# Kernel optimization log

Measured on AMD Instinct MI355X. Metric: run time of the kernel, lower is better.

## Reference

```python
import jax, jax.numpy as jnp
import numpy as np

B, D, O = 32768, 512, 16          # batch, input_size, output_size
E, K, T = 16, 4, 3                # n_expert, top-k, n_task
H1, H2 = 16, 8                    # Expert hidden sizes (hard-coded in Expert)
SPARSE_COEF, OLMO_COEF, RZ_COEF = 0.01, 0.01, 0.001


def setup_inputs() -> dict:
    key = jax.random.key(0)
    ks = jax.random.split(key, 8)
    s = 0.05
    return {
        "x": jax.random.normal(ks[0], (B, D), jnp.float32),
        # per-task gate params (torch inits zeros; random here for a meaningful test)
        "w_gates": jax.random.normal(ks[1], (T, D, E), jnp.float32) * s,
        "b_gates": jnp.zeros((T, E), jnp.float32),
        # stacked expert MLP params: Linear(D,16)->ReLU->Linear(16,8)->ReLU->Linear(8,O)->ReLU
        "W1": jax.random.normal(ks[2], (E, D, H1), jnp.float32) * s,
        "b1": jnp.zeros((E, H1), jnp.float32),
        "W2": jax.random.normal(ks[3], (E, H1, H2), jnp.float32) * s,
        "b2": jnp.zeros((E, H2), jnp.float32),
        "W3": jax.random.normal(ks[4], (E, H2, O), jnp.float32) * s,
        "b3": jnp.zeros((E, O), jnp.float32),
    }


def cv_squared(v):
    # torch .var() is unbiased (ddof=1)
    eps = 1e-10
    return jnp.var(v, ddof=1) / (jnp.mean(v) ** 2 + eps)


def reference(x, w_gates, b_gates, W1, b1, W2, b2, W3, b3):
    Bn = x.shape[0]
    # router z loss uses raw input x (as in the source)
    rz_per_task = jnp.sum(jax.nn.logsumexp(x, axis=-1)) / Bn

    # All experts on all samples, vectorized over the expert axis.
    # (experts are identical across tasks, so compute once; gating makes it sparse)
    h1 = jax.nn.relu(jnp.einsum('bd,edh->ebh', x, W1) + b1[:, None, :])   # [E,B,16]
    h2 = jax.nn.relu(jnp.einsum('ebh,ehk->ebk', h1, W2) + b2[:, None, :])  # [E,B,8]
    eo = jax.nn.relu(jnp.einsum('ebk,eko->ebo', h2, W3) + b3[:, None, :])  # [E,B,O]

    row = jnp.arange(Bn)[:, None]
    ys = []
    lb_loss = jnp.float32(0.0)
    rz_loss = jnp.float32(0.0)
    for t in range(T):  # small fixed task loop
        logits = x @ w_gates[t] + b_gates[t]               # [B,E]
        top_vals, top_idx = jax.lax.top_k(logits, K)
        top_gates = jax.nn.softmax(top_vals, axis=1)
        gates = jnp.zeros_like(logits).at[row, top_idx].set(top_gates)  # [B,E]

        load = (gates > 0).sum(0).astype(jnp.float32)      # eval-mode load
        importance = gates.sum(0)
        sparse_lb = cv_squared(importance) + cv_squared(load)
        olmo_lb = E * jnp.sum(importance * (load / Bn))
        lb_loss = lb_loss + sparse_lb * SPARSE_COEF + olmo_lb * OLMO_COEF
        rz_loss = rz_loss + rz_per_task * RZ_COEF

        # combine: y[b] = sum_e gates[b,e] * expert_e(x[b])
        ys.append(jnp.einsum('be,ebo->bo', gates, eo))
    return (jnp.stack(ys), lb_loss, rz_loss)
```

## Files before the change

### kernel.cpp

```cpp
#include <hip/hip_runtime.h>
#include <hip/hip_bf16.h>

#define BSZ 32768
#define TT  3
#define OO  16

typedef __attribute__((ext_vector_type(8))) short bf16x8;
typedef __attribute__((ext_vector_type(4))) float f32x4;

__device__ __forceinline__ float bf2f(unsigned short u) {
  return __uint_as_float(((unsigned)u) << 16);
}
__device__ __forceinline__ unsigned short f2bf(float f) {
  unsigned u = __float_as_uint(f);
  u += 0x7fffu + ((u >> 16) & 1u);
  return (unsigned short)(u >> 16);
}
__device__ __forceinline__ unsigned pack2(unsigned short a, unsigned short b) {
  return (unsigned)a | ((unsigned)b << 16);
}

__global__ void k_prepw(const float* __restrict__ W1, const float* __restrict__ wg,
                        unsigned short* __restrict__ Wfh,
                        unsigned short* __restrict__ Wfl, float* __restrict__ acc) {
  if (blockIdx.x == 0 && threadIdx.x < 97) acc[threadIdx.x] = 0.f;
  for (int idx = blockIdx.x * 256 + threadIdx.x; idx < 20 * 16 * 64 * 8;
       idx += gridDim.x * 256) {
    const int nblk = idx >> 13, itg = (idx >> 9) & 15;
    const int lane = (idx >> 3) & 63, j = idx & 7;
    const int n = nblk * 16 + (lane & 15);
    const int k = itg * 32 + (lane >> 4) * 8 + j;
    float v = 0.f;
    if (n < 256) v = W1[(size_t)(n >> 4) * 8192 + k * 16 + (n & 15)];
    else if (n < 304) v = wg[(size_t)((n - 256) >> 4) * 8192 + k * 16 + ((n - 256) & 15)];
    const unsigned short hi = f2bf(v);
    Wfh[idx] = hi;
    Wfl[idx] = f2bf(v - bf2f(hi));
  }
}

struct FSmem {
  union {
    struct {
      unsigned short xh[4][4][64][8];
      unsigned short xl[4][4][64][8];
    } a;
    struct {
      unsigned short hd[16][264];
      float eoL[16][16][17];
      float gvL[64][12];
      int   giL[64][12];
      union {
        float lgs[64][52];
        struct { float W2t[2048], W3t[2048]; } t;
      } u2;
      float b2t[128], b3t[256];
      float impL[48], loadL[48];
      int   nresc, resc[192];
      double resL[16];
    } b;
  } u;
  float rzrow[64];
};

__global__ __launch_bounds__(512, 4) void k_fused(
    const float* __restrict__ x, const unsigned short* __restrict__ Wfh,
    const unsigned short* __restrict__ Wfl, const float* __restrict__ b1,
    const float* __restrict__ bg, const float* __restrict__ wg,
    const float* __restrict__ W2, const float* __restrict__ b2,
    const float* __restrict__ W3, const float* __restrict__ b3,
    float* __restrict__ out, float* __restrict__ acc_imp,
    float* __restrict__ acc_load, float* __restrict__ rz_acc) {
  __shared__ FSmem sm;
  const int tid = threadIdx.x;
  const int b0 = blockIdx.x * 64;
  const int w = tid >> 6, l = tid & 63;
  const int l15 = l & 15, quad = l >> 4;
  const int mh = w >> 2;
  const int cg = w & 3;
  const int srow = tid >> 3, skf = tid & 7;
  const int sm_abs = srow >> 4;
  const int slane = (srow & 15) + 16 * (skf >> 1);
  const int sj = (skf & 1) * 4;

  f32x4 acc[2][5];
#pragma unroll
  for (int m = 0; m < 2; m++)
#pragma unroll
    for (int c = 0; c < 5; c++) acc[m][c] = (f32x4){0.f, 0.f, 0.f, 0.f};
  float rzsum = 0.f;

  auto woffs = [&](int itg, int c) -> size_t {
    return ((size_t)(((cg * 5 + c) * 16 + itg) * 64 + l)) * 8;
  };

#pragma unroll 1
  for (int ch = 0; ch < 4; ++ch) {
    if (ch) __syncthreads();
    {
      float4 xv[4];
      const float* xp = &x[(size_t)(b0 + srow) * 512 + ch * 128 + skf * 4];
#pragma unroll
      for (int r = 0; r < 4; r++) xv[r] = *(const float4*)(xp + r * 32);
#pragma unroll
      for (int r = 0; r < 4; r++) {
        const float v0 = xv[r].x, v1 = xv[r].y, v2 = xv[r].z, v3 = xv[r].w;
        rzsum += __expf(v0) + __expf(v1) + __expf(v2) + __expf(v3);
        const unsigned short h0 = f2bf(v0), h1_ = f2bf(v1), h2_ = f2bf(v2), h3 = f2bf(v3);
        uint2 ph, pl;
        ph.x = pack2(h0, h1_); ph.y = pack2(h2_, h3);
        pl.x = pack2(f2bf(v0 - bf2f(h0)), f2bf(v1 - bf2f(h1_)));
        pl.y = pack2(f2bf(v2 - bf2f(h2_)), f2bf(v3 - bf2f(h3)));
        *(uint2*)&sm.u.a.xh[sm_abs][r][slane][sj] = ph;
        *(uint2*)&sm.u.a.xl[sm_abs][r][slane][sj] = pl;
      }
    }
    __syncthreads();

    bf16x8 bh = *(const bf16x8*)&Wfh[woffs(ch * 4, 0)];
    bf16x8 bl = *(const bf16x8*)&Wfl[woffs(ch * 4, 0)];
#pragma unroll
    for (int it = 0; it < 4; ++it) {
      bf16x8 ah[2], al[2];
#pragma unroll
      for (int m = 0; m < 2; m++) {
        ah[m] = *(const bf16x8*)&sm.u.a.xh[mh * 2 + m][it][l][0];
        al[m] = *(const bf16x8*)&sm.u.a.xl[mh * 2 + m][it][l][0];
      }
#pragma unroll
      for (int c = 0; c < 5; c++) {
        bf16x8 bhn = bh, bln = bl;
        if (!((it == 3) && (c == 4))) {
          const int nit = (c == 4) ? it + 1 : it;
          const int nc  = (c == 4) ? 0 : c + 1;
          const size_t o = woffs(ch * 4 + nit, nc);
          bhn = *(const bf16x8*)&Wfh[o];
          bln = *(const bf16x8*)&Wfl[o];
        }
#pragma unroll
        for (int m = 0; m < 2; m++) {
          acc[m][c] = __builtin_amdgcn_mfma_f32_16x16x32_bf16(ah[m], bh, acc[m][c], 0, 0, 0);
          acc[m][c] = __builtin_amdgcn_mfma_f32_16x16x32_bf16(al[m], bh, acc[m][c], 0, 0, 0);
          acc[m][c] = __builtin_amdgcn_mfma_f32_16x16x32_bf16(ah[m], bl, acc[m][c], 0, 0, 0);
        }
        bh = bhn; bl = bln;
      }
    }
  }

  rzsum += __shfl_xor(rzsum, 1);
  rzsum += __shfl_xor(rzsum, 2);
  rzsum += __shfl_xor(rzsum, 4);
  if (skf == 0) sm.rzrow[srow] = rzsum;
  __syncthreads();

  if (tid < 64) {
    float vv = __logf(sm.rzrow[tid]);
#pragma unroll
    for (int off = 32; off; off >>= 1) vv += __shfl_xor(vv, off);
    if (tid == 0) atomicAdd(rz_acc, vv);
  }
  if (cg == 3) {
#pragma unroll
    for (int c = 1; c < 4; c++) {
      const int cc = 16 * c + l15 - 16;
#pragma unroll
      for (int m = 0; m < 2; m++)
#pragma unroll
        for (int reg = 0; reg < 4; reg++) {
          const int row = 32 * mh + 16 * m + quad * 4 + reg;
          sm.u.b.u2.lgs[row][cc] = acc[m][c][reg] + bg[cc];
        }
    }
  }
  if (tid < 48) { sm.u.b.impL[tid] = 0.f; sm.u.b.loadL[tid] = 0.f; }
  if (tid == 0) sm.u.b.nresc = 0;
  __syncthreads();

  if (tid < 192) {
    const int r = tid & 63, tk = tid >> 6;
    float v[16];
#pragma unroll
    for (int e = 0; e < 16; e++) v[e] = sm.u.b.u2.lgs[r][tk * 16 + e];
    unsigned used = 0;
    int idx[5]; float val[5];
#pragma unroll
    for (int p = 0; p < 5; p++) {
      float best = -INFINITY; int bi = 0;
#pragma unroll
      for (int e = 0; e < 16; e++) {
        const float ve = ((used >> e) & 1u) ? -INFINITY : v[e];
        if (ve > best) { best = ve; bi = e; }
      }
      idx[p] = bi; val[p] = best; used |= 1u << bi;
    }
    if (val[3] - val[4] < 3e-3f) {
      const int s = atomicAdd(&sm.u.b.nresc, 1);
      sm.u.b.resc[s] = (r << 2) | tk;
    }
    const float m = val[0];
    float ex[4], sum = 0.f;
#pragma unroll
    for (int p = 0; p < 4; p++) { ex[p] = __expf(val[p] - m); sum += ex[p]; }
#pragma unroll
    for (int p = 0; p < 4; p++) {
      const float g = ex[p] / sum;
      sm.u.b.gvL[r][tk * 4 + p] = g;
      sm.u.b.giL[r][tk * 4 + p] = idx[p];
      atomicAdd(&sm.u.b.impL[tk * 16 + idx[p]], g);
      atomicAdd(&sm.u.b.loadL[tk * 16 + idx[p]], 1.f);
    }
  }
  __syncthreads();

  const int nr = sm.u.b.nresc;
  for (int i = 0; i < nr; i++) {
    const int st = sm.u.b.resc[i];
    const int r = st >> 2, tk = st & 3;
    if (tid < 256) {
      const int e = tid >> 4, part = tid & 15;
      const float* xr2 = &x[(size_t)(b0 + r) * 512];
      const float* wgc = &wg[(size_t)tk * 8192 + e];
      double a = 0.0;
      for (int d = part * 32; d < part * 32 + 32; d++)
        a += (double)xr2[d] * (double)wgc[(size_t)d * 16];
#pragma unroll
      for (int off = 1; off < 16; off <<= 1) a += __shfl_xor(a, off);
      if (part == 0) sm.u.b.resL[e] = a + (double)bg[tk * 16 + e];
    }
    __syncthreads();
    if (tid == 0) {
      for (int p = 0; p < 4; p++) {
        sm.u.b.impL[tk * 16 + sm.u.b.giL[r][tk * 4 + p]] -= sm.u.b.gvL[r][tk * 4 + p];
        sm.u.b.loadL[tk * 16 + sm.u.b.giL[r][tk * 4 + p]] -= 1.f;
      }
      unsigned used = 0;
      int idx[4]; float val[4];
      for (int p = 0; p < 4; p++) {
        double best = -1e300; int bi = 0;
        for (int e2 = 0; e2 < 16; e2++) {
          if ((used >> e2) & 1u) continue;
          const double ve = sm.u.b.resL[e2];
          if (ve > best) { best = ve; bi = e2; }
        }
        idx[p] = bi; val[p] = (float)best; used |= 1u << bi;
      }
      const float m = val[0];
      float ex[4], sum = 0.f;
      for (int p = 0; p < 4; p++) { ex[p] = __expf(val[p] - m); sum += ex[p]; }
      for (int p = 0; p < 4; p++) {
        const float g = ex[p] / sum;
        sm.u.b.gvL[r][tk * 4 + p] = g;
        sm.u.b.giL[r][tk * 4 + p] = idx[p];
        sm.u.b.impL[tk * 16 + idx[p]] += g;
        sm.u.b.loadL[tk * 16 + idx[p]] += 1.f;
      }
    }
    __syncthreads();
  }
  if (tid < 48) {
    atomicAdd(&acc_imp[tid], sm.u.b.impL[tid]);
    atomicAdd(&acc_load[tid], sm.u.b.loadL[tid]);
  }

  for (int d = tid; d < 2048; d += 512) {
    sm.u.b.u2.t.W2t[(d & 127) * 16 + (d >> 7)] = W2[d];
    sm.u.b.u2.t.W3t[(d & 127) * 16 + (d >> 7)] = W3[d];
  }
  if (tid < 128) sm.u.b.b2t[(tid & 7) * 16 + (tid >> 3)] = b2[tid];
  if (tid < 256) sm.u.b.b3t[(tid & 15) * 16 + (tid >> 4)] = b3[tid];
  __syncthreads();

#pragma unroll
  for (int ch = 0; ch < 4; ++ch) {
    if (mh == (ch >> 1)) {
      const int m = ch & 1;
#pragma unroll
      for (int c = 0; c < 5; c++) {
        const int col = 80 * cg + 16 * c + l15;
        if (col < 256) {
#pragma unroll
          for (int reg = 0; reg < 4; reg++)
            sm.u.b.hd[quad * 4 + reg][col] = f2bf(fmaxf(acc[m][c][reg] + b1[col], 0.f));
        }
      }
    }
    __syncthreads();
    if (tid < 256) {
      const int e = tid & 15, sr = tid >> 4;
      float h1v[16];
#pragma unroll
      for (int q = 0; q < 4; q++) {
        const ushort4 uu = *(const ushort4*)&sm.u.b.hd[sr][e * 16 + q * 4];
        h1v[q * 4 + 0] = bf2f(uu.x);
        h1v[q * 4 + 1] = bf2f(uu.y);
        h1v[q * 4 + 2] = bf2f(uu.z);
        h1v[q * 4 + 3] = bf2f(uu.w);
      }
      float h2v[8];
#pragma unroll
      for (int j = 0; j < 8; j++) {
        float a = sm.u.b.b2t[j * 16 + e];
#pragma unroll
        for (int k = 0; k < 16; k++) a += h1v[k] * sm.u.b.u2.t.W2t[(k * 8 + j) * 16 + e];
        h2v[j] = fmaxf(a, 0.f);
      }
#pragma unroll
      for (int o = 0; o < 16; o++) {
        float a = sm.u.b.b3t[o * 16 + e];
#pragma unroll
        for (int j = 0; j < 8; j++) a += h2v[j] * sm.u.b.u2.t.W3t[(j * 16 + o) * 16 + e];
        sm.u.b.eoL[sr][e][o] = fmaxf(a, 0.f);
      }
    }
    __syncthreads();
    if (tid < 256) {
      const int o = tid & 15, sr = tid >> 4;
      const int rl = ch * 16 + sr;
#pragma unroll
      for (int tk = 0; tk < TT; tk++) {
        float y = 0.f;
#pragma unroll
        for (int p = 0; p < 4; p++)
          y += sm.u.b.gvL[rl][tk * 4 + p] * sm.u.b.eoL[sr][sm.u.b.giL[rl][tk * 4 + p]][o];
        out[((size_t)tk * BSZ + b0 + rl) * OO + o] = y;
      }
    }
    __syncthreads();
  }
}

__global__ void k_final(const float* __restrict__ acc_imp,
                        const float* __restrict__ acc_load,
                        const float* __restrict__ rz_acc,
                        float* __restrict__ out_tail) {
  if (threadIdx.x == 0 && blockIdx.x == 0) {
    double lb = 0.0;
    for (int t = 0; t < TT; t++) {
      const float* imp = &acc_imp[t * 16];
      const float* ld = &acc_load[t * 16];
      double si = 0, sl = 0, dot = 0;
      for (int e2 = 0; e2 < 16; e2++) {
        si += imp[e2]; sl += ld[e2]; dot += (double)imp[e2] * ld[e2];
      }
      const double mi = si / 16.0, ml = sl / 16.0;
      double vi = 0, vl = 0;
      for (int e2 = 0; e2 < 16; e2++) {
        const double di = imp[e2] - mi, dl = ld[e2] - ml;
        vi += di * di; vl += dl * dl;
      }
      vi /= 15.0; vl /= 15.0;
      lb += (vi / (mi * mi + 1e-10) + vl / (ml * ml + 1e-10)) * 0.01
          + 16.0 * dot / (double)BSZ * 0.01;
    }
    out_tail[0] = (float)lb;
    out_tail[1] = (float)(3.0 * (rz_acc[0] / (double)BSZ) * 0.001);
  }
}

extern "C" void kernel_launch(void* const* d_in, const int* in_sizes, int n_in,
                              void* d_out, int out_size, void* d_ws, size_t ws_size,
                              hipStream_t stream) {
  const float* x  = (const float*)d_in[0];
  const float* wg = (const float*)d_in[1];
  const float* bg = (const float*)d_in[2];
  const float* W1 = (const float*)d_in[3];
  const float* b1 = (const float*)d_in[4];
  const float* W2 = (const float*)d_in[5];
  const float* b2 = (const float*)d_in[6];
  const float* W3 = (const float*)d_in[7];
  const float* b3 = (const float*)d_in[8];
  float* out = (float*)d_out;

  char* wsb = (char*)d_ws;
  unsigned short* Wfh = (unsigned short*)wsb;
  unsigned short* Wfl = (unsigned short*)(wsb + 327680);
  float* acc = (float*)(wsb + 655360);

  k_prepw<<<dim3(640), dim3(256), 0, stream>>>(W1, wg, Wfh, Wfl, acc);
  k_fused<<<dim3(BSZ / 64), dim3(512), 0, stream>>>(
      x, Wfh, Wfl, b1, bg, wg, W2, b2, W3, b3, out, acc, acc + 48, acc + 96);
  k_final<<<dim3(1), dim3(64), 0, stream>>>(acc, acc + 48, acc + 96,
                                            out + (size_t)TT * BSZ * OO);
}
```

Measured before the change: 234.5 us.

## Switch to fp16 split-x MFMA, MFMA expert tail, fuse final reduction

The main GEMM now uses fp16: x is split into hi/lo fp16 parts, while weights are rounded to a single fp16 copy. This needs 2 MFMAs per tile instead of 3 bf16 ones and halves weight traffic. The per-expert 16->8->16 MLP tail moves from scalar LDS loops to small 16x16x16 fp16 MFMAs on the accumulator registers, with swizzled eoL storage. The next x chunk is prefetched into registers, and the separate finalize kernel is folded into the last block through an atomic counter. The rescue threshold is tightened. Risks are accuracy loss from the single fp16 weight rounding and fp16 range limits.

```diff
diff --git a/kernel.cpp b/kernel.cpp
--- a/kernel.cpp
+++ b/kernel.cpp
@@ -1,29 +1,30 @@
 #include <hip/hip_runtime.h>
-#include <hip/hip_bf16.h>
 
 #define BSZ 32768
 #define TT  3
 #define OO  16
-
-typedef __attribute__((ext_vector_type(8))) short bf16x8;
+#define RESCUE_THR 2.5e-3f
+
+typedef __attribute__((ext_vector_type(8))) _Float16 f16x8;
+typedef __attribute__((ext_vector_type(4))) _Float16 f16x4;
 typedef __attribute__((ext_vector_type(4))) float f32x4;
 
-__device__ __forceinline__ float bf2f(unsigned short u) {
-  return __uint_as_float(((unsigned)u) << 16);
-}
-__device__ __forceinline__ unsigned short f2bf(float f) {
-  unsigned u = __float_as_uint(f);
-  u += 0x7fffu + ((u >> 16) & 1u);
-  return (unsigned short)(u >> 16);
+__device__ __forceinline__ unsigned short f2h(float f) {
+  return __builtin_bit_cast(unsigned short, (_Float16)f);
+}
+__device__ __forceinline__ float h2f(unsigned short u) {
+  return (float)__builtin_bit_cast(_Float16, u);
 }
 __device__ __forceinline__ unsigned pack2(unsigned short a, unsigned short b) {
   return (unsigned)a | ((unsigned)b << 16);
 }
 
 __global__ void k_prepw(const float* __restrict__ W1, const float* __restrict__ wg,
-                        unsigned short* __restrict__ Wfh,
-                        unsigned short* __restrict__ Wfl, float* __restrict__ acc) {
-  if (blockIdx.x == 0 && threadIdx.x < 97) acc[threadIdx.x] = 0.f;
+                        const float* __restrict__ W2, const float* __restrict__ W3,
+                        unsigned short* __restrict__ Wf,
+                        unsigned short* __restrict__ W2A,
+                        unsigned short* __restrict__ W3A, float* __restrict__ acc) {
+  if (blockIdx.x == 0 && threadIdx.x < 98) acc[threadIdx.x] = 0.f;
   for (int idx = blockIdx.x * 256 + threadIdx.x; idx < 20 * 16 * 64 * 8;
        idx += gridDim.x * 256) {
     const int nblk = idx >> 13, itg = (idx >> 9) & 15;
@@ -33,9 +34,14 @@
     float v = 0.f;
     if (n < 256) v = W1[(size_t)(n >> 4) * 8192 + k * 16 + (n & 15)];
     else if (n < 304) v = wg[(size_t)((n - 256) >> 4) * 8192 + k * 16 + ((n - 256) & 15)];
-    const unsigned short hi = f2bf(v);
-    Wfh[idx] = hi;
-    Wfl[idx] = f2bf(v - bf2f(hi));
+    Wf[idx] = f2h(v);
+  }
+  const int idx2 = blockIdx.x * 256 + threadIdx.x;
+  if (idx2 < 16 * 64 * 4) {
+    const int e = idx2 >> 8, lane = (idx2 >> 2) & 63, j = idx2 & 3;
+    const int m = lane & 15, k = (lane >> 4) * 4 + j;
+    W2A[idx2] = f2h((m < 8) ? W2[e * 128 + k * 8 + m] : 0.f);
+    W3A[idx2] = f2h((k < 8) ? W3[e * 128 + k * 16 + m] : 0.f);
   }
 }
 
@@ -46,15 +52,12 @@
       unsigned short xl[4][4][64][8];
     } a;
     struct {
-      unsigned short hd[16][264];
-      float eoL[16][16][17];
+      union {
+        float lgs[64][52];
+        float eoL[2][16][16][16];
+      } u2;
       float gvL[64][12];
       int   giL[64][12];
-      union {
-        float lgs[64][52];
-        struct { float W2t[2048], W3t[2048]; } t;
-      } u2;
-      float b2t[128], b3t[256];
       float impL[48], loadL[48];
       int   nresc, resc[192];
       double resL[16];
@@ -64,13 +67,12 @@
 };
 
 __global__ __launch_bounds__(512, 4) void k_fused(
-    const float* __restrict__ x, const unsigned short* __restrict__ Wfh,
-    const unsigned short* __restrict__ Wfl, const float* __restrict__ b1,
-    const float* __restrict__ bg, const float* __restrict__ wg,
-    const float* __restrict__ W2, const float* __restrict__ b2,
-    const float* __restrict__ W3, const float* __restrict__ b3,
-    float* __restrict__ out, float* __restrict__ acc_imp,
-    float* __restrict__ acc_load, float* __restrict__ rz_acc) {
+    const float* __restrict__ x, const unsigned short* __restrict__ Wf,
+    const float* __restrict__ b1, const float* __restrict__ bg,
+    const float* __restrict__ wg, const unsigned short* __restrict__ W2A,
+    const float* __restrict__ b2, const unsigned short* __restrict__ W3A,
+    const float* __restrict__ b3, float* __restrict__ out, float* acc_imp,
+    float* acc_load, float* rz_acc, unsigned* ctr) {
   __shared__ FSmem sm;
   const int tid = threadIdx.x;
   const int b0 = blockIdx.x * 64;
@@ -94,57 +96,56 @@
     return ((size_t)(((cg * 5 + c) * 16 + itg) * 64 + l)) * 8;
   };
 
+  const float* xbase = &x[(size_t)(b0 + srow) * 512 + skf * 4];
+  float4 xv[4];
+#pragma unroll
+  for (int r = 0; r < 4; r++) xv[r] = *(const float4*)(xbase + r * 32);
+
 #pragma unroll 1
   for (int ch = 0; ch < 4; ++ch) {
     if (ch) __syncthreads();
     {
-      float4 xv[4];
-      const float* xp = &x[(size_t)(b0 + srow) * 512 + ch * 128 + skf * 4];
-#pragma unroll
-      for (int r = 0; r < 4; r++) xv[r] = *(const float4*)(xp + r * 32);
 #pragma unroll
       for (int r = 0; r < 4; r++) {
         const float v0 = xv[r].x, v1 = xv[r].y, v2 = xv[r].z, v3 = xv[r].w;
         rzsum += __expf(v0) + __expf(v1) + __expf(v2) + __expf(v3);
-        const unsigned short h0 = f2bf(v0), h1_ = f2bf(v1), h2_ = f2bf(v2), h3 = f2bf(v3);
+        const unsigned short h0 = f2h(v0), h1_ = f2h(v1), h2_ = f2h(v2), h3 = f2h(v3);
         uint2 ph, pl;
         ph.x = pack2(h0, h1_); ph.y = pack2(h2_, h3);
-        pl.x = pack2(f2bf(v0 - bf2f(h0)), f2bf(v1 - bf2f(h1_)));
-        pl.y = pack2(f2bf(v2 - bf2f(h2_)), f2bf(v3 - bf2f(h3)));
+        pl.x = pack2(f2h(v0 - h2f(h0)), f2h(v1 - h2f(h1_)));
+        pl.y = pack2(f2h(v2 - h2f(h2_)), f2h(v3 - h2f(h3)));
         *(uint2*)&sm.u.a.xh[sm_abs][r][slane][sj] = ph;
         *(uint2*)&sm.u.a.xl[sm_abs][r][slane][sj] = pl;
       }
     }
     __syncthreads();
 
-    bf16x8 bh = *(const bf16x8*)&Wfh[woffs(ch * 4, 0)];
-    bf16x8 bl = *(const bf16x8*)&Wfl[woffs(ch * 4, 0)];
-#pragma unroll
-    for (int it = 0; it < 4; ++it) {
-      bf16x8 ah[2], al[2];
+    f16x8 bh0 = *(const f16x8*)&Wf[woffs(ch * 4, 0)];
+    f16x8 bh1 = *(const f16x8*)&Wf[woffs(ch * 4, 1)];
+    if (ch < 3) {
+#pragma unroll
+      for (int r = 0; r < 4; r++)
+        xv[r] = *(const float4*)(xbase + (ch + 1) * 128 + r * 32);
+    }
+    f16x8 ah[2], al[2];
+#pragma unroll
+    for (int i = 0; i < 20; ++i) {
+      const int it = i / 5, c = i % 5;
+      if (c == 0) {
+#pragma unroll
+        for (int m = 0; m < 2; m++) {
+          ah[m] = *(const f16x8*)&sm.u.a.xh[mh * 2 + m][it][l][0];
+          al[m] = *(const f16x8*)&sm.u.a.xl[mh * 2 + m][it][l][0];
+        }
+      }
+      f16x8 bh2 = bh0;
+      if (i + 2 < 20) bh2 = *(const f16x8*)&Wf[woffs(ch * 4 + (i + 2) / 5, (i + 2) % 5)];
 #pragma unroll
       for (int m = 0; m < 2; m++) {
-        ah[m] = *(const bf16x8*)&sm.u.a.xh[mh * 2 + m][it][l][0];
-        al[m] = *(const bf16x8*)&sm.u.a.xl[mh * 2 + m][it][l][0];
-      }
-#pragma unroll
-      for (int c = 0; c < 5; c++) {
-        bf16x8 bhn = bh, bln = bl;
-        if (!((it == 3) && (c == 4))) {
-          const int nit = (c == 4) ? it + 1 : it;
-          const int nc  = (c == 4) ? 0 : c + 1;
-          const size_t o = woffs(ch * 4 + nit, nc);
-          bhn = *(const bf16x8*)&Wfh[o];
-          bln = *(const bf16x8*)&Wfl[o];
-        }
-#pragma unroll
-        for (int m = 0; m < 2; m++) {
-          acc[m][c] = __builtin_amdgcn_mfma_f32_16x16x32_bf16(ah[m], bh, acc[m][c], 0, 0, 0);
-          acc[m][c] = __builtin_amdgcn_mfma_f32_16x16x32_bf16(al[m], bh, acc[m][c], 0, 0, 0);
-          acc[m][c] = __builtin_amdgcn_mfma_f32_16x16x32_bf16(ah[m], bl, acc[m][c], 0, 0, 0);
-        }
-        bh = bhn; bl = bln;
-      }
+        acc[m][c] = __builtin_amdgcn_mfma_f32_16x16x32_f16(bh0, ah[m], acc[m][c], 0, 0, 0);
+        acc[m][c] = __builtin_amdgcn_mfma_f32_16x16x32_f16(bh0, al[m], acc[m][c], 0, 0, 0);
+      }
+      bh0 = bh1; bh1 = bh2;
     }
   }
 
@@ -163,12 +164,12 @@
   if (cg == 3) {
 #pragma unroll
     for (int c = 1; c < 4; c++) {
-      const int cc = 16 * c + l15 - 16;
 #pragma unroll
       for (int m = 0; m < 2; m++)
 #pragma unroll
         for (int reg = 0; reg < 4; reg++) {
-          const int row = 32 * mh + 16 * m + quad * 4 + reg;
+          const int row = 32 * mh + 16 * m + l15;
+          const int cc = 16 * (c - 1) + quad * 4 + reg;
           sm.u.b.u2.lgs[row][cc] = acc[m][c][reg] + bg[cc];
         }
     }
@@ -194,7 +195,7 @@
       }
       idx[p] = bi; val[p] = best; used |= 1u << bi;
     }
-    if (val[3] - val[4] < 3e-3f) {
+    if (val[3] - val[4] < RESCUE_THR) {
       const int s = atomicAdd(&sm.u.b.nresc, 1);
       sm.u.b.resc[s] = (r << 2) | tk;
     }
@@ -263,98 +264,80 @@
     atomicAdd(&acc_load[tid], sm.u.b.loadL[tid]);
   }
 
-  for (int d = tid; d < 2048; d += 512) {
-    sm.u.b.u2.t.W2t[(d & 127) * 16 + (d >> 7)] = W2[d];
-    sm.u.b.u2.t.W3t[(d & 127) * 16 + (d >> 7)] = W3[d];
-  }
-  if (tid < 128) sm.u.b.b2t[(tid & 7) * 16 + (tid >> 3)] = b2[tid];
-  if (tid < 256) sm.u.b.b3t[(tid & 15) * 16 + (tid >> 4)] = b3[tid];
-  __syncthreads();
-
-#pragma unroll
-  for (int ch = 0; ch < 4; ++ch) {
-    if (mh == (ch >> 1)) {
-      const int m = ch & 1;
-#pragma unroll
-      for (int c = 0; c < 5; c++) {
-        const int col = 80 * cg + 16 * c + l15;
-        if (col < 256) {
-#pragma unroll
-          for (int reg = 0; reg < 4; reg++)
-            sm.u.b.hd[quad * 4 + reg][col] = f2bf(fmaxf(acc[m][c][reg] + b1[col], 0.f));
-        }
+  const int nexp = (cg < 3) ? 5 : 1;
+#pragma unroll 1
+  for (int m = 0; m < 2; ++m) {
+    if (m) __syncthreads();
+#pragma unroll
+    for (int c = 0; c < 5; ++c) {
+      if (c < nexp) {
+        const int e = 5 * cg + c;
+        const f32x4 b1v = *(const f32x4*)&b1[(e << 4) + quad * 4];
+        f16x4 h1f;
+#pragma unroll
+        for (int r = 0; r < 4; r++)
+          h1f[r] = (_Float16)fmaxf(acc[m][c][r] + b1v[r], 0.f);
+        const f16x4 w2 = *(const f16x4*)&W2A[((size_t)e * 64 + l) * 4];
+        f32x4 h2 = (quad < 2) ? *(const f32x4*)&b2[e * 8 + quad * 4]
+                              : (f32x4){0.f, 0.f, 0.f, 0.f};
+        h2 = __builtin_amdgcn_mfma_f32_16x16x16f16(w2, h1f, h2, 0, 0, 0);
+        f16x4 h2q;
+#pragma unroll
+        for (int r = 0; r < 4; r++) h2q[r] = (_Float16)fmaxf(h2[r], 0.f);
+        const f16x4 w3 = *(const f16x4*)&W3A[((size_t)e * 64 + l) * 4];
+        f32x4 eo = *(const f32x4*)&b3[(e << 4) + quad * 4];
+        eo = __builtin_amdgcn_mfma_f32_16x16x16f16(w3, h2q, eo, 0, 0, 0);
+#pragma unroll
+        for (int r = 0; r < 4; r++) eo[r] = fmaxf(eo[r], 0.f);
+        *(f32x4*)&sm.u.b.u2.eoL[mh][l15][e][(quad * 4) ^ ((l15 & 3) << 2)] = eo;
       }
     }
     __syncthreads();
-    if (tid < 256) {
-      const int e = tid & 15, sr = tid >> 4;
-      float h1v[16];
-#pragma unroll
-      for (int q = 0; q < 4; q++) {
-        const ushort4 uu = *(const ushort4*)&sm.u.b.hd[sr][e * 16 + q * 4];
-        h1v[q * 4 + 0] = bf2f(uu.x);
-        h1v[q * 4 + 1] = bf2f(uu.y);
-        h1v[q * 4 + 2] = bf2f(uu.z);
-        h1v[q * 4 + 3] = bf2f(uu.w);
-      }
-      float h2v[8];
-#pragma unroll
-      for (int j = 0; j < 8; j++) {
-        float a = sm.u.b.b2t[j * 16 + e];
-#pragma unroll
-        for (int k = 0; k < 16; k++) a += h1v[k] * sm.u.b.u2.t.W2t[(k * 8 + j) * 16 + e];
-        h2v[j] = fmaxf(a, 0.f);
-      }
-#pragma unroll
-      for (int o = 0; o < 16; o++) {
-        float a = sm.u.b.b3t[o * 16 + e];
-#pragma unroll
-        for (int j = 0; j < 8; j++) a += h2v[j] * sm.u.b.u2.t.W3t[(j * 16 + o) * 16 + e];
-        sm.u.b.eoL[sr][e][o] = fmaxf(a, 0.f);
-      }
-    }
-    __syncthreads();
-    if (tid < 256) {
-      const int o = tid & 15, sr = tid >> 4;
-      const int rl = ch * 16 + sr;
+    {
+      const int rid = tid >> 4, o = tid & 15;
+      const int mh_r = rid >> 4, r16 = rid & 15;
+      const int rl = 32 * mh_r + 16 * m + r16;
+      const int osw = (r16 & 3) << 2;
 #pragma unroll
       for (int tk = 0; tk < TT; tk++) {
         float y = 0.f;
 #pragma unroll
         for (int p = 0; p < 4; p++)
-          y += sm.u.b.gvL[rl][tk * 4 + p] * sm.u.b.eoL[sr][sm.u.b.giL[rl][tk * 4 + p]][o];
+          y += sm.u.b.gvL[rl][tk * 4 + p] *
+               sm.u.b.u2.eoL[mh_r][r16][sm.u.b.giL[rl][tk * 4 + p]][o ^ osw];
         out[((size_t)tk * BSZ + b0 + rl) * OO + o] = y;
       }
     }
-    __syncthreads();
-  }
-}
-
-__global__ void k_final(const float* __restrict__ acc_imp,
-                        const float* __restrict__ acc_load,
-                        const float* __restrict__ rz_acc,
-                        float* __restrict__ out_tail) {
-  if (threadIdx.x == 0 && blockIdx.x == 0) {
-    double lb = 0.0;
-    for (int t = 0; t < TT; t++) {
-      const float* imp = &acc_imp[t * 16];
-      const float* ld = &acc_load[t * 16];
-      double si = 0, sl = 0, dot = 0;
-      for (int e2 = 0; e2 < 16; e2++) {
-        si += imp[e2]; sl += ld[e2]; dot += (double)imp[e2] * ld[e2];
-      }
-      const double mi = si / 16.0, ml = sl / 16.0;
-      double vi = 0, vl = 0;
-      for (int e2 = 0; e2 < 16; e2++) {
-        const double di = imp[e2] - mi, dl = ld[e2] - ml;
-        vi += di * di; vl += dl * dl;
-      }
-      vi /= 15.0; vl /= 15.0;
-      lb += (vi / (mi * mi + 1e-10) + vl / (ml * ml + 1e-10)) * 0.01
-          + 16.0 * dot / (double)BSZ * 0.01;
-    }
-    out_tail[0] = (float)lb;
-    out_tail[1] = (float)(3.0 * (rz_acc[0] / (double)BSZ) * 0.001);
+  }
+
+  __syncthreads();
+  if (tid == 0) {
+    __threadfence();
+    const unsigned done = atomicAdd(ctr, 1u);
+    if (done == gridDim.x - 1) {
+      __threadfence();
+      double lb = 0.0;
+      for (int t = 0; t < TT; t++) {
+        const float* imp = &acc_imp[t * 16];
+        const float* ld = &acc_load[t * 16];
+        double si = 0, sl = 0, dot = 0;
+        for (int e2 = 0; e2 < 16; e2++) {
+          si += imp[e2]; sl += ld[e2]; dot += (double)imp[e2] * ld[e2];
+        }
+        const double mi = si / 16.0, ml = sl / 16.0;
+        double vi = 0, vl = 0;
+        for (int e2 = 0; e2 < 16; e2++) {
+          const double di = imp[e2] - mi, dl = ld[e2] - ml;
+          vi += di * di; vl += dl * dl;
+        }
+        vi /= 15.0; vl /= 15.0;
+        lb += (vi / (mi * mi + 1e-10) + vl / (ml * ml + 1e-10)) * 0.01
+            + 16.0 * dot / (double)BSZ * 0.01;
+      }
+      float* out_tail = out + (size_t)TT * BSZ * OO;
+      out_tail[0] = (float)lb;
+      out_tail[1] = (float)(3.0 * (rz_acc[0] / (double)BSZ) * 0.001);
+    }
   }
 }
 
@@ -373,13 +356,13 @@
   float* out = (float*)d_out;
 
   char* wsb = (char*)d_ws;
-  unsigned short* Wfh = (unsigned short*)wsb;
-  unsigned short* Wfl = (unsigned short*)(wsb + 327680);
-  float* acc = (float*)(wsb + 655360);
-
-  k_prepw<<<dim3(640), dim3(256), 0, stream>>>(W1, wg, Wfh, Wfl, acc);
+  unsigned short* Wf  = (unsigned short*)wsb;
+  unsigned short* W2A = (unsigned short*)(wsb + 327680);
+  unsigned short* W3A = (unsigned short*)(wsb + 335872);
+  float* acc = (float*)(wsb + 344064);
+
+  k_prepw<<<dim3(640), dim3(256), 0, stream>>>(W1, wg, W2, W3, Wf, W2A, W3A, acc);
   k_fused<<<dim3(BSZ / 64), dim3(512), 0, stream>>>(
-      x, Wfh, Wfl, b1, bg, wg, W2, b2, W3, b3, out, acc, acc + 48, acc + 96);
-  k_final<<<dim3(1), dim3(64), 0, stream>>>(acc, acc + 48, acc + 96,
-                                            out + (size_t)TT * BSZ * OO);
-}
+      x, Wf, b1, bg, wg, W2A, b2, W3A, b3, out, acc, acc + 48, acc + 96,
+      (unsigned*)(acc + 97));
+}
```

Result: slower. 249.5 us (+6.4%).
